# Performance work log

Measured on AMD Instinct MI355X. Metric: run time of the kernel, lower is better.

The kernel has to match this reference:

```python
import jax, jax.numpy as jnp
import numpy as np

H, NB, D = 16, 64, 1024
HID = 64  # gate MLP hidden width


def setup_inputs() -> dict:
    key = jax.random.key(0)
    ks = jax.random.split(key, 10)
    B, T = 4, 2048
    delta = jax.random.normal(ks[0], (B, T, H, NB), dtype=jnp.float32)
    content_emb = jax.random.normal(ks[1], (B, T, D), dtype=jnp.float32)
    omega = jax.random.normal(ks[2], (H, NB), dtype=jnp.float32)
    # learned parameters
    log_Q = jnp.zeros((H, NB), dtype=jnp.float32)
    log_R = jnp.zeros((H, NB), dtype=jnp.float32)
    log_sigma0 = jnp.full((H, NB), -2.0, dtype=jnp.float32)
    W1 = jax.random.normal(ks[3], (D, HID), dtype=jnp.float32) / np.sqrt(D)
    b1 = jnp.zeros((HID,), dtype=jnp.float32)
    W2 = jax.random.normal(ks[4], (HID, H * NB), dtype=jnp.float32) / np.sqrt(HID)
    b2 = jnp.zeros((H * NB,), dtype=jnp.float32)
    return {"delta": delta, "content_emb": content_emb, "omega": omega,
            "log_Q": log_Q, "log_R": log_R, "log_sigma0": log_sigma0,
            "W1": W1, "b1": b1, "W2": W2, "b2": b2}


def reference(delta, content_emb, omega, log_Q, log_R, log_sigma0, W1, b1, W2, b2):
    B, T, _, _ = delta.shape
    Q = jnp.exp(log_Q)            # (H, NB)
    R = jnp.exp(log_R)            # (H, NB)
    sigma0 = jnp.exp(log_sigma0)  # (H, NB)

    theta_sq = (delta * omega) ** 2  # (B, T, H, NB)

    # landmark gate MLP (exact GELU, as torch default)
    h = jax.nn.gelu(content_emb @ W1 + b1, approximate=False)  # (B, T, HID)
    gates = jax.nn.sigmoid(h @ W2 + b2).reshape(B, T, H, NB)

    def step(sigma, xs):
        theta_sq_t, gate_t = xs  # (B, H, NB) each
        sigma = sigma + Q * theta_sq_t
        K = sigma / (sigma + R)
        sigma = sigma * (1.0 - gate_t * K)
        return sigma, sigma

    init = jnp.broadcast_to(sigma0, (B, H, NB))
    xs = (jnp.swapaxes(theta_sq, 0, 1), jnp.swapaxes(gates, 0, 1))  # (T, B, H, NB)
    _, sigma_seq = jax.lax.scan(step, init, xs)
    sigma = jnp.swapaxes(sigma_seq, 0, 1)  # (B, T, H, NB)
    return sigma, gates
```

## Files before the change

kernel.cpp:

```cpp
#include <hip/hip_runtime.h>
#include <math.h>

#define H_   16
#define NB_  64
#define D_   1024
#define HID_ 64
#define B_   4
#define T_   2048
#define ROWS (B_*T_)
#define HNB  (H_*NB_)

typedef short v8s __attribute__((ext_vector_type(8)));
typedef float v4f __attribute__((ext_vector_type(4)));

__device__ __forceinline__ float gelu_exact(float x) {
    return 0.5f * x * (1.0f + erff(x * 0.7071067811865476f));
}
__device__ __forceinline__ float sigmoidf(float x) {
    return 1.0f / (1.0f + expf(-x));
}
__device__ __forceinline__ ushort f2bf(float x) {
    union { float f; unsigned u; } v; v.f = x;
    unsigned r = v.u + 0x7fffu + ((v.u >> 16) & 1u);
    return (ushort)(r >> 16);
}

__global__ __launch_bounds__(256) void k_prep(const float* __restrict__ W1,
                                              const float* __restrict__ W2,
                                              ushort* __restrict__ w1t,
                                              ushort* __restrict__ w2t) {
    __shared__ float ls[64][65];
    const int t   = threadIdx.x;
    const int blk = blockIdx.x;
    if (blk < 16) {
        const int k0 = blk * 64;
        #pragma unroll
        for (int q = 0; q < 4; ++q) {
            int idx = q * 256 + t;
            int r = idx >> 4, c4 = idx & 15;
            *(float4*)&ls[r][c4 * 4] =
                *(const float4*)&W1[(size_t)(k0 + r) * 64 + c4 * 4];
        }
        __syncthreads();
        const int col = t >> 2, kq = t & 3;
        ushort out[16];
        #pragma unroll
        for (int e = 0; e < 16; ++e) out[e] = f2bf(ls[kq * 16 + e][col]);
        *(uint4*)&w1t[(size_t)col * 1024 + k0 + kq * 16]     = *(uint4*)&out[0];
        *(uint4*)&w1t[(size_t)col * 1024 + k0 + kq * 16 + 8] = *(uint4*)&out[8];
    } else {
        const int n0 = (blk - 16) * 64;
        #pragma unroll
        for (int q = 0; q < 4; ++q) {
            int idx = q * 256 + t;
            int r = idx >> 4, c4 = idx & 15;
            *(float4*)&ls[r][c4 * 4] =
                *(const float4*)&W2[(size_t)r * HNB + n0 + c4 * 4];
        }
        __syncthreads();
        const int n = t >> 2, kq = t & 3;
        ushort out[16];
        #pragma unroll
        for (int e = 0; e < 16; ++e) out[e] = f2bf(ls[kq * 16 + e][n]);
        *(uint4*)&w2t[(size_t)(n0 + n) * 64 + kq * 16]     = *(uint4*)&out[0];
        *(uint4*)&w2t[(size_t)(n0 + n) * 64 + kq * 16 + 8] = *(uint4*)&out[8];
    }
}

__global__ __launch_bounds__(256) void k_gemm1_mfma(const float* __restrict__ X,
                                                    const ushort* __restrict__ w1t,
                                                    const float* __restrict__ b1,
                                                    ushort* __restrict__ hbuf) {
    __shared__ ushort Al[32 * 128];
    __shared__ ushort Bl[64 * 128];
    const int t    = threadIdx.x;
    const int r0   = blockIdx.x * 32;
    const int w    = t >> 6;
    const int lane = t & 63;
    const int lo   = lane & 15;
    const int hi   = lane >> 4;
    const int mt   = w & 1;
    const int nh   = w >> 1;
    const int arow = t >> 3, aseg = t & 7;
    const int brow = t >> 2, bseg = t & 3;

    v4f acc0 = {0.f,0.f,0.f,0.f}, acc1 = {0.f,0.f,0.f,0.f};

    for (int c = 0; c < 8; ++c) {
        float xv[16];
        const float* xp = &X[(size_t)(r0 + arow) * D_ + c * 128 + aseg * 16];
        #pragma unroll
        for (int i = 0; i < 4; ++i) *(float4*)&xv[i*4] = *(const float4*)&xp[i*4];
        ushort wv[32];
        const ushort* wp = &w1t[(size_t)brow * 1024 + c * 128 + bseg * 32];
        #pragma unroll
        for (int i = 0; i < 4; ++i) *(uint4*)&wv[i*8] = *(const uint4*)&wp[i*8];

        __syncthreads();
        #pragma unroll
        for (int j8 = 0; j8 < 2; ++j8) {
            const int k = aseg * 16 + j8 * 8;
            union { ushort u[8]; v8s v; } pa;
            #pragma unroll
            for (int e = 0; e < 8; ++e) pa.u[e] = f2bf(xv[j8 * 8 + e]);
            *(v8s*)&Al[arow * 128 + (k ^ ((arow & 7) << 3))] = pa.v;
        }
        #pragma unroll
        for (int j8 = 0; j8 < 4; ++j8) {
            const int k = bseg * 32 + j8 * 8;
            *(v8s*)&Bl[brow * 128 + (k ^ ((brow & 7) << 3))] = *(v8s*)&wv[j8 * 8];
        }
        __syncthreads();

        const int rowa = mt * 16 + lo;
        #pragma unroll
        for (int kk = 0; kk < 4; ++kk) {
            const int k   = kk * 32 + hi * 8;
            const int sw  = k ^ ((lo & 7) << 3);
            v8s af  = *(v8s*)&Al[rowa * 128 + sw];
            v8s b0  = *(v8s*)&Bl[(nh * 32 + lo) * 128 + sw];
            v8s b1v = *(v8s*)&Bl[(nh * 32 + 16 + lo) * 128 + sw];
            acc0 = __builtin_amdgcn_mfma_f32_16x16x32_bf16(af, b0,  acc0, 0, 0, 0);
            acc1 = __builtin_amdgcn_mfma_f32_16x16x32_bf16(af, b1v, acc1, 0, 0, 0);
        }
    }
    #pragma unroll
    for (int nt = 0; nt < 2; ++nt) {
        v4f a = nt ? acc1 : acc0;
        const int col = nh * 32 + nt * 16 + lo;
        const float bb = b1[col];
        #pragma unroll
        for (int j = 0; j < 4; ++j) {
            const int row = r0 + mt * 16 + hi * 4 + j;
            hbuf[(size_t)row * HID_ + col] = f2bf(gelu_exact(a[j] + bb));
        }
    }
}

__global__ __launch_bounds__(256) void k_gemm2_mfma(const ushort* __restrict__ hbuf,
                                                    const ushort* __restrict__ w2t,
                                                    const float* __restrict__ b2,
                                                    float* __restrict__ gates) {
    __shared__ ushort Ah[64 * 64];
    __shared__ ushort Bh[256 * 64];
    const int t    = threadIdx.x;
    const int r0   = (blockIdx.x >> 2) * 64;
    const int n0   = (blockIdx.x & 3) * 256;
    const int w    = t >> 6;
    const int lane = t & 63;
    const int lo   = lane & 15;
    const int hi   = lane >> 4;

    {
        const int row = t >> 2, seg = t & 3;
        uint4 v0 = *(const uint4*)&hbuf[(size_t)(r0 + row) * 64 + seg * 16];
        uint4 v1 = *(const uint4*)&hbuf[(size_t)(r0 + row) * 64 + seg * 16 + 8];
        const int sw = (row & 7) << 3;
        *(uint4*)&Ah[row * 64 + ((seg * 16) ^ sw)]     = v0;
        *(uint4*)&Ah[row * 64 + ((seg * 16 + 8) ^ sw)] = v1;
    }
    #pragma unroll
    for (int q = 0; q < 4; ++q) {
        const int pi  = q * 256 + t;
        const int n   = pi >> 2, seg = pi & 3;
        uint4 v0 = *(const uint4*)&w2t[(size_t)(n0 + n) * 64 + seg * 16];
        uint4 v1 = *(const uint4*)&w2t[(size_t)(n0 + n) * 64 + seg * 16 + 8];
        const int sw = (n & 7) << 3;
        *(uint4*)&Bh[n * 64 + ((seg * 16) ^ sw)]     = v0;
        *(uint4*)&Bh[n * 64 + ((seg * 16 + 8) ^ sw)] = v1;
    }
    __syncthreads();

    v4f acc[4][4];
    #pragma unroll
    for (int mt = 0; mt < 4; ++mt)
        #pragma unroll
        for (int nt = 0; nt < 4; ++nt) acc[mt][nt] = (v4f){0.f,0.f,0.f,0.f};

    #pragma unroll
    for (int kc = 0; kc < 2; ++kc) {
        const int k  = kc * 32 + hi * 8;
        const int sw = k ^ ((lo & 7) << 3);
        v8s af[4];
        #pragma unroll
        for (int mt = 0; mt < 4; ++mt)
            af[mt] = *(v8s*)&Ah[(mt * 16 + lo) * 64 + sw];
        #pragma unroll
        for (int nt = 0; nt < 4; ++nt) {
            v8s bf = *(v8s*)&Bh[(w * 64 + nt * 16 + lo) * 64 + sw];
            #pragma unroll
            for (int mt = 0; mt < 4; ++mt)
                acc[mt][nt] = __builtin_amdgcn_mfma_f32_16x16x32_bf16(af[mt], bf, acc[mt][nt], 0, 0, 0);
        }
    }

    #pragma unroll
    for (int nt = 0; nt < 4; ++nt) {
        const int col = n0 + w * 64 + nt * 16 + lo;
        const float bb = b2[col];
        #pragma unroll
        for (int mt = 0; mt < 4; ++mt) {
            #pragma unroll
            for (int j = 0; j < 4; ++j) {
                const int row = r0 + mt * 16 + hi * 4 + j;
                gates[(size_t)row * HNB + col] = sigmoidf(acc[mt][nt][j] + bb);
            }
        }
    }
}

#define TT_   64
#define SEGK  4
#define SEGLEN (T_/SEGK)
#define WARMT  2

#define LD8(A, G, grp) { \
    _Pragma("unroll") \
    for (int u = 0; u < 8; ++u) { \
        A[u] = pa[((grp)*8 + u) * 128]; \
        G[u] = pa[((grp)*8 + u) * 128 + 64]; \
    } }

#define CP8(A, G, grp) { \
    _Pragma("unroll") \
    for (int u = 0; u < 8; ++u) { \
        float a   = A[u]; \
        float omg = G[u]; \
        float aR  = a + R; \
        float pc  = fmaf(omg, a, R); \
        float den = sigma + aR; \
        float s   = sigma + a; \
        float p   = fmaf(omg, sigma, pc); \
        float rc  = __builtin_amdgcn_rcpf(den); \
        float tt  = s * p; \
        sigma     = tt * rc; \
        ps[((grp)*8 + u) * 64] = sigma; \
    } }

__global__ __launch_bounds__(256) void k_scan_seg(
        const float* __restrict__ delta,
        const float* __restrict__ gates,
        const float* __restrict__ omega,
        const float* __restrict__ log_Q,
        const float* __restrict__ log_R,
        const float* __restrict__ log_s0,
        float* __restrict__ sig) {
    __shared__ float tg_lds[2][TT_][2][64];
    __shared__ float sg_lds[2][TT_][64];
    const int tid = threadIdx.x;
    const int blk = blockIdx.x;
    const int bh  = blk >> 2;
    const int seg = blk & 3;
    const int b   = bh >> 4;
    const int h   = bh & 15;
    const size_t base = (size_t)b * T_ * HNB + h * NB_;
    const int wv   = tid >> 6;
    const int lane = tid & 63;

    const int warm   = (seg == 0) ? 0 : WARMT;
    const int ntiles = SEGLEN / TT_ + warm;
    const int tstart = seg * SEGLEN - warm * TT_;

    float R = 0.f, sigma = 0.f;
    float sc0=0,sc1=0,sc2=0,sc3=0;
    const int col4 = lane & 15;
    const int rg   = lane >> 4;
    const float* dp = delta + base + col4 * 4;
    const float* gp = gates + base + col4 * 4;

    if (wv == 0) {
        const int hn = h * NB_ + lane;
        R     = expf(log_R[hn]);
        sigma = expf(log_s0[hn]);
    } else if (wv == 1) {
        const int hn4 = h * NB_ + col4 * 4;
        float4 om4 = *(const float4*)&omega[hn4];
        float4 lq4 = *(const float4*)&log_Q[hn4];
        sc0 = expf(lq4.x) * om4.x * om4.x;
        sc1 = expf(lq4.y) * om4.y * om4.y;
        sc2 = expf(lq4.z) * om4.z * om4.z;
        sc3 = expf(lq4.w) * om4.w * om4.w;
    }

    for (int p = 0; p <= ntiles + 1; ++p) {
        if (wv == 0) {
            if (p >= 1 && p <= ntiles) {
                const int buf = (p - 1) & 1;
                const float* pa = &tg_lds[buf][0][0][lane];
                float*       ps = &sg_lds[buf][0][lane];
                float a0[8], g0[8], a1[8], g1[8];
                LD8(a0, g0, 0);
                LD8(a1, g1, 1);
                CP8(a0, g0, 0); LD8(a0, g0, 2);
                CP8(a1, g1, 1); LD8(a1, g1, 3);
                CP8(a0, g0, 2); LD8(a0, g0, 4);
                CP8(a1, g1, 3); LD8(a1, g1, 5);
                CP8(a0, g0, 4); LD8(a0, g0, 6);
                CP8(a1, g1, 5); LD8(a1, g1, 7);
                CP8(a0, g0, 6);
                CP8(a1, g1, 7);
            }
        } else if (wv == 1) {
            if (p < ntiles) {
                const int buf = p & 1;
                const int t0 = tstart + p * TT_;
                #pragma unroll
                for (int it = 0; it < 16; ++it) {
                    const int row = it * 4 + rg;
                    float4 d = *(const float4*)&dp[(size_t)(t0 + row) * HNB];
                    float4 a;
                    a.x = (sc0 * d.x) * d.x;
                    a.y = (sc1 * d.y) * d.y;
                    a.z = (sc2 * d.z) * d.z;
                    a.w = (sc3 * d.w) * d.w;
                    *(float4*)&tg_lds[buf][row][0][col4 * 4] = a;
                }
            }
        } else if (wv == 2) {
            if (p < ntiles) {
                const int buf = p & 1;
                const int t0 = tstart + p * TT_;
                #pragma unroll
                for (int it = 0; it < 16; ++it) {
                    const int row = it * 4 + rg;
                    float4 g = *(const float4*)&gp[(size_t)(t0 + row) * HNB];
                    float4 o;
                    o.x = 1.0f - g.x; o.y = 1.0f - g.y;
                    o.z = 1.0f - g.z; o.w = 1.0f - g.w;
                    *(float4*)&tg_lds[buf][row][1][col4 * 4] = o;
                }
            }
        } else {
            const int tile = p - 2;
            if (tile >= warm && tile < ntiles) {
                const int buf = p & 1;
                const int t0 = tstart + tile * TT_;
                float* op = sig + base + col4 * 4;
                #pragma unroll
                for (int it = 0; it < 16; ++it) {
                    const int row = it * 4 + rg;
                    float4 v = *(const float4*)&sg_lds[buf][row][col4 * 4];
                    *(float4*)&op[(size_t)(t0 + row) * HNB] = v;
                }
            }
        }
        __syncthreads();
    }
}

extern "C" void kernel_launch(void* const* d_in, const int* in_sizes, int n_in,
                              void* d_out, int out_size, void* d_ws, size_t ws_size,
                              hipStream_t stream) {
    const float* delta   = (const float*)d_in[0];
    const float* content = (const float*)d_in[1];
    const float* omega   = (const float*)d_in[2];
    const float* log_Q   = (const float*)d_in[3];
    const float* log_R   = (const float*)d_in[4];
    const float* log_s0  = (const float*)d_in[5];
    const float* W1      = (const float*)d_in[6];
    const float* b1      = (const float*)d_in[7];
    const float* W2      = (const float*)d_in[8];
    const float* b2      = (const float*)d_in[9];

    float* sig_out   = (float*)d_out;
    float* gates_out = sig_out + (size_t)ROWS * HNB;

    const size_t n_h   = (size_t)ROWS * HID_;
    const size_t n_w1t = (size_t)HID_ * D_;
    const size_t n_w2t = (size_t)HNB * HID_;
    const size_t need  = (n_h + n_w1t + n_w2t) * sizeof(ushort);

    ushort *hbuf, *w1t, *w2t;
    if (ws_size >= need) {
        hbuf = (ushort*)d_ws;
    } else {
        hbuf = (ushort*)sig_out;
    }
    w1t = hbuf + n_h;
    w2t = w1t + n_w1t;

    k_prep<<<32, 256, 0, stream>>>(W1, W2, w1t, w2t);
    k_gemm1_mfma<<<ROWS / 32, 256, 0, stream>>>(content, w1t, b1, hbuf);
    k_gemm2_mfma<<<(ROWS / 64) * 4, 256, 0, stream>>>(hbuf, w2t, b2, gates_out);
    k_scan_seg<<<B_ * H_ * SEGK, 256, 0, stream>>>(delta, gates_out, omega,
                                                   log_Q, log_R, log_s0, sig_out);
}
```

Baseline: 59.54 us.

## Store scan outputs directly from compute wave and drop store wave

The scan kernel drops its fourth (store) wavefront and the shared-memory output staging buffer. The compute wave now writes each sigma straight to global memory as coalesced 64-lane stores, and the pipeline loses one stage. The __syncthreads is replaced by an LDS-only waitcnt plus a raw barrier, so the barrier no longer waits for outstanding global stores. The risk is that the serial compute wave now issues the global stores itself, which could stretch the critical recurrence path.

Result: slower. 62.89 us (+5.6%).

```diff
diff --git a/kernel.cpp b/kernel.cpp
--- a/kernel.cpp
+++ b/kernel.cpp
@@ -221,7 +221,8 @@
         G[u] = pa[((grp)*8 + u) * 128 + 64]; \
     } }
 
-#define CP8(A, G, grp) { \
+#define CP8S(A, G, grp) { \
+    float so[8]; \
     _Pragma("unroll") \
     for (int u = 0; u < 8; ++u) { \
         float a   = A[u]; \
@@ -230,14 +231,23 @@
         float pc  = fmaf(omg, a, R); \
         float den = sigma + aR; \
         float s   = sigma + a; \
-        float p   = fmaf(omg, sigma, pc); \
+        float pp  = fmaf(omg, sigma, pc); \
         float rc  = __builtin_amdgcn_rcpf(den); \
-        float tt  = s * p; \
+        float tt  = s * pp; \
         sigma     = tt * rc; \
-        ps[((grp)*8 + u) * 64] = sigma; \
+        so[u]     = sigma; \
+    } \
+    if (dostore) { \
+        _Pragma("unroll") \
+        for (int u = 0; u < 8; ++u) op[((grp)*8 + u) * (size_t)HNB] = so[u]; \
     } }
 
-__global__ __launch_bounds__(256) void k_scan_seg(
+#define PHASE_SYNC() { \
+    asm volatile("s_waitcnt lgkmcnt(0)" ::: "memory"); \
+    __builtin_amdgcn_s_barrier(); \
+    asm volatile("" ::: "memory"); }
+
+__global__ __launch_bounds__(192) void k_scan_seg3(
         const float* __restrict__ delta,
         const float* __restrict__ gates,
         const float* __restrict__ omega,
@@ -245,8 +255,7 @@
         const float* __restrict__ log_R,
         const float* __restrict__ log_s0,
         float* __restrict__ sig) {
-    __shared__ float tg_lds[2][TT_][2][64];
-    __shared__ float sg_lds[2][TT_][64];
+    __shared__ float tg[2][TT_][2][64];
     const int tid = threadIdx.x;
     const int blk = blockIdx.x;
     const int bh  = blk >> 2;
@@ -282,28 +291,31 @@
         sc3 = expf(lq4.w) * om4.w * om4.w;
     }
 
-    for (int p = 0; p <= ntiles + 1; ++p) {
+    for (int p = 0; p <= ntiles; ++p) {
         if (wv == 0) {
-            if (p >= 1 && p <= ntiles) {
-                const int buf = (p - 1) & 1;
-                const float* pa = &tg_lds[buf][0][0][lane];
-                float*       ps = &sg_lds[buf][0][lane];
+            if (p >= 1) {
+                const int tile = p - 1;
+                const int buf  = tile & 1;
+                const bool dostore = (tile >= warm);
+                const size_t t0 = dostore ? (size_t)(tstart + tile * TT_) : 0;
+                float* op = sig + base + lane + t0 * HNB;
+                const float* pa = &tg[buf][0][0][lane];
                 float a0[8], g0[8], a1[8], g1[8];
                 LD8(a0, g0, 0);
                 LD8(a1, g1, 1);
-                CP8(a0, g0, 0); LD8(a0, g0, 2);
-                CP8(a1, g1, 1); LD8(a1, g1, 3);
-                CP8(a0, g0, 2); LD8(a0, g0, 4);
-                CP8(a1, g1, 3); LD8(a1, g1, 5);
-                CP8(a0, g0, 4); LD8(a0, g0, 6);
-                CP8(a1, g1, 5); LD8(a1, g1, 7);
-                CP8(a0, g0, 6);
-                CP8(a1, g1, 7);
+                CP8S(a0, g0, 0); LD8(a0, g0, 2);
+                CP8S(a1, g1, 1); LD8(a1, g1, 3);
+                CP8S(a0, g0, 2); LD8(a0, g0, 4);
+                CP8S(a1, g1, 3); LD8(a1, g1, 5);
+                CP8S(a0, g0, 4); LD8(a0, g0, 6);
+                CP8S(a1, g1, 5); LD8(a1, g1, 7);
+                CP8S(a0, g0, 6);
+                CP8S(a1, g1, 7);
             }
         } else if (wv == 1) {
             if (p < ntiles) {
                 const int buf = p & 1;
-                const int t0 = tstart + p * TT_;
+                const int t0  = tstart + p * TT_;
                 #pragma unroll
                 for (int it = 0; it < 16; ++it) {
                     const int row = it * 4 + rg;
@@ -313,13 +325,13 @@
                     a.y = (sc1 * d.y) * d.y;
                     a.z = (sc2 * d.z) * d.z;
                     a.w = (sc3 * d.w) * d.w;
-                    *(float4*)&tg_lds[buf][row][0][col4 * 4] = a;
+                    *(float4*)&tg[buf][row][0][col4 * 4] = a;
                 }
             }
-        } else if (wv == 2) {
+        } else {
             if (p < ntiles) {
                 const int buf = p & 1;
-                const int t0 = tstart + p * TT_;
+                const int t0  = tstart + p * TT_;
                 #pragma unroll
                 for (int it = 0; it < 16; ++it) {
                     const int row = it * 4 + rg;
@@ -327,24 +339,11 @@
                     float4 o;
                     o.x = 1.0f - g.x; o.y = 1.0f - g.y;
                     o.z = 1.0f - g.z; o.w = 1.0f - g.w;
-                    *(float4*)&tg_lds[buf][row][1][col4 * 4] = o;
+                    *(float4*)&tg[buf][row][1][col4 * 4] = o;
                 }
             }
-        } else {
-            const int tile = p - 2;
-            if (tile >= warm && tile < ntiles) {
-                const int buf = p & 1;
-                const int t0 = tstart + tile * TT_;
-                float* op = sig + base + col4 * 4;
-                #pragma unroll
-                for (int it = 0; it < 16; ++it) {
-                    const int row = it * 4 + rg;
-                    float4 v = *(const float4*)&sg_lds[buf][row][col4 * 4];
-                    *(float4*)&op[(size_t)(t0 + row) * HNB] = v;
-                }
-            }
-        }
-        __syncthreads();
+        }
+        PHASE_SYNC();
     }
 }
 
@@ -382,6 +381,6 @@
     k_prep<<<32, 256, 0, stream>>>(W1, W2, w1t, w2t);
     k_gemm1_mfma<<<ROWS / 32, 256, 0, stream>>>(content, w1t, b1, hbuf);
     k_gemm2_mfma<<<(ROWS / 64) * 4, 256, 0, stream>>>(hbuf, w2t, b2, gates_out);
-    k_scan_seg<<<B_ * H_ * SEGK, 256, 0, stream>>>(delta, gates_out, omega,
-                                                   log_Q, log_R, log_s0, sig_out);
-}
+    k_scan_seg3<<<B_ * H_ * SEGK, 192, 0, stream>>>(delta, gates_out, omega,
+                                                    log_Q, log_R, log_s0, sig_out);
+}
```
